# Optimization experiments

Measured on AMD Instinct MI355X. Metric: run time of the kernel, lower is better.

The kernel has to match this reference:

```python
import jax, jax.numpy as jnp
import numpy as np

NUM_CLASSES = 5  # config['training']['num_classes_per_task']


def _conv(x, w, b):
    # x: [N,C,H,W], w: [O,I,kh,kw] (torch OIHW), valid padding, stride 1
    y = jax.lax.conv_general_dilated(
        x, w, window_strides=(1, 1), padding='VALID',
        dimension_numbers=('NCHW', 'OIHW', 'NCHW'))
    return y + b[None, :, None, None]


def _maxpool2(x):
    return jax.lax.reduce_window(x, -jnp.inf, jax.lax.max,
                                 (1, 1, 2, 2), (1, 1, 2, 2), 'VALID')


def _lenet(x, c1w, c1b, c2w, c2b, f1w, f1b, f2w, f2b, f3w, f3b):
    h = _maxpool2(jax.nn.relu(_conv(x, c1w, c1b)))   # [N,6,14,14]
    h = _maxpool2(jax.nn.relu(_conv(h, c2w, c2b)))   # [N,16,5,5]
    h = h.reshape(h.shape[0], -1)                     # [N,400]
    h = jax.nn.relu(h @ f1w.T + f1b)                  # [N,120]
    h = jax.nn.relu(h @ f2w.T + f2b)                  # [N,84]
    return h @ f3w.T + f3b                            # [N,64] embeddings


def setup_inputs() -> dict:
    key = jax.random.key(0)
    ks = jax.random.split(key, 7)
    def w(k, shape, fan_in):
        return jax.random.normal(k, shape, jnp.float32) * (1.0 / np.sqrt(fan_in))
    return {
        'x': jax.random.normal(ks[0], (20480, 3, 32, 32), jnp.float32),
        'c1w': w(ks[1], (6, 3, 5, 5), 3 * 25), 'c1b': jnp.zeros((6,), jnp.float32),
        'c2w': w(ks[2], (16, 6, 5, 5), 6 * 25), 'c2b': jnp.zeros((16,), jnp.float32),
        'f1w': w(ks[3], (120, 400), 400), 'f1b': jnp.zeros((120,), jnp.float32),
        'f2w': w(ks[4], (84, 120), 120), 'f2b': jnp.zeros((84,), jnp.float32),
        'f3w': w(ks[5], (64, 84), 84), 'f3b': jnp.zeros((64,), jnp.float32),
    }


def reference(x, c1w, c1b, c2w, c2b, f1w, f1b, f2w, f2b, f3w, f3b):
    emb = _lenet(x, c1w, c1b, c2w, c2b, f1w, f1b, f2w, f2b, f3w, f3b)  # [N,64]
    # prototypes = embeddings.sum() / num_classes  (scalar, as in source)
    proto = emb.sum() / NUM_CLASSES
    result = jax.nn.softmax(emb, axis=1)
    # sqrt((result - proto)^2) elementwise == |result - proto|; the python
    # per-sample list-comprehension just rebuilds this same [N,64] tensor.
    return jnp.sqrt(jnp.square(result - proto))
```

## Files before the change

kernel.cpp:

```cpp
#include <hip/hip_runtime.h>
#include <math.h>

typedef __attribute__((ext_vector_type(8))) short short8;
typedef __attribute__((ext_vector_type(4))) float f32x4;
typedef __attribute__((ext_vector_type(4))) unsigned short us4v;

__device__ __forceinline__ unsigned short f2bf(float f) {
    unsigned u = __float_as_uint(f);
    return (unsigned short)((u + 0x7FFFu + ((u >> 16) & 1u)) >> 16);
}
__device__ __forceinline__ unsigned cvtpk(float lo, float hi) {
    unsigned r;
    asm("v_cvt_pk_bf16_f32 %0, %1, %2" : "=v"(r) : "v"(lo), "v"(hi));
    return r;
}
__device__ __forceinline__ unsigned short f2bf1(float v) {
    return (unsigned short)(cvtpk(v, 0.f) & 0xffffu);
}
__device__ __forceinline__ float fmax_x8(float v) {
    int s = __builtin_amdgcn_mov_dpp(__float_as_int(v), 0x128, 0xf, 0xf, true);
    return fmaxf(v, __int_as_float(s));
}

#define C1T_SS 3464
#define C1_RS 36
#define P1R 1176

__global__ __launch_bounds__(256, 3) void conv12_mfma(
    const float* __restrict__ x,
    const unsigned short* __restrict__ c1wf, const float* __restrict__ c1b,
    const unsigned short* __restrict__ c2wf, const float* __restrict__ c2b,
    unsigned short* __restrict__ P2)
{
    __shared__ __align__(16) unsigned short img[2 * C1T_SS];
    __shared__ __align__(16) unsigned short p1s[16 * P1R + 16];
    const int t = threadIdx.x;
    const int lane = t & 63, w = t >> 6;
    const int grp = lane >> 4, c = lane & 15;
    const int smp = c >> 3, q = c & 7;

    if (t < 192) {
        int s = t / 96, rr = t - s * 96;
        *(uint2*)&img[s * C1T_SS + rr * C1_RS + 32] = make_uint2(0u, 0u);
    }
    if (t < 2) {
        *(uint4*)&img[t * C1T_SS + 3456] = make_uint4(0u, 0u, 0u, 0u);
        *(uint4*)&p1s[16 * P1R + t * 8] = make_uint4(0u, 0u, 0u, 0u);
    }

    short8 wf1[5][4];
#pragma unroll
    for (int s = 0; s < 5; s++)
#pragma unroll
        for (int off = 0; off < 4; off++)
            wf1[s][off] = *(const short8*)&c1wf[(((s * 4 + off) * 4 + grp) * 16 + c) * 8];
    int ciA[5], kpA[5];
#pragma unroll
    for (int s = 0; s < 5; s++) {
        int b = s * 4 + grp; if (b > 17) b = 17;
        ciA[s] = b / 6; kpA[s] = b % 6;
    }
    const float bias1 = (c < 6) ? c1b[c] : 0.f;

    const float4* xs4 = (const float4*)(x + (size_t)blockIdx.x * 49152);
    float4 r[6];

#pragma unroll
    for (int k = 0; k < 6; k++) r[k] = xs4[k * 256 + t];

    for (int st = 0; st < 8; st++) {
#pragma unroll
        for (int k = 0; k < 6; k++) {
            int f = k * 256 + t;
            int s = (f >= 768) ? 1 : 0;
            int w4 = f - s * 768;
            int ci = w4 >> 8, rem = w4 & 255, y = rem >> 3, xq = rem & 7;
            uint2 pk = make_uint2(cvtpk(r[k].x, r[k].y), cvtpk(r[k].z, r[k].w));
            *(uint2*)&img[s * C1T_SS + (ci * 32 + y) * C1_RS + xq * 4] = pk;
        }
        __syncthreads();

        if (st < 7) {
#pragma unroll
            for (int k = 0; k < 6; k++) r[k] = xs4[(st + 1) * 1536 + k * 256 + t];
        }

        for (int py = w; py < 14; py += 4) {
            f32x4 a00 = {0.f,0.f,0.f,0.f}, a01 = a00, a10 = a00, a11 = a00;
#pragma unroll
            for (int s = 0; s < 5; s++) {
                int e = smp * C1T_SS + (ciA[s] * 32 + py * 2 + kpA[s]) * C1_RS + q * 4;
                union { us4v h[2]; short8 v; } af;
                af.h[0] = *(const us4v*)&img[e];
                af.h[1] = *(const us4v*)&img[e + 4];
                a00 = __builtin_amdgcn_mfma_f32_16x16x32_bf16(af.v, wf1[s][0], a00, 0, 0, 0);
                a01 = __builtin_amdgcn_mfma_f32_16x16x32_bf16(af.v, wf1[s][1], a01, 0, 0, 0);
                a10 = __builtin_amdgcn_mfma_f32_16x16x32_bf16(af.v, wf1[s][2], a10, 0, 0, 0);
                a11 = __builtin_amdgcn_mfma_f32_16x16x32_bf16(af.v, wf1[s][3], a11, 0, 0, 0);
            }
            f32x4 pe2, po2;
#pragma unroll
            for (int i = 0; i < 4; i++) {
                pe2[i] = fmax_x8(fmaxf(a00[i], a01[i]));
                po2[i] = fmax_x8(fmaxf(a10[i], a11[i]));
            }
            if (c < 6) {
#pragma unroll
                for (int i = 0; i < 4; i++) {
                    int m = grp * 4 + i;
                    int qo = m & 7;
                    if (qo < 7) {
                        int sm = m >> 3;
                        float v0 = fmaxf(pe2[i] + bias1, 0.f);
                        float v1 = fmaxf(po2[i] + bias1, 0.f);
                        *(unsigned*)&p1s[(2 * st + sm) * P1R + (c * 14 + py) * 14 + qo * 2]
                            = cvtpk(v0, v1);
                    }
                }
            }
        }
        __syncthreads();
    }

    short8 wf2[8][2];
#pragma unroll
    for (int s = 0; s < 8; s++)
#pragma unroll
        for (int off = 0; off < 2; off++)
            wf2[s][off] = *(const short8*)&c2wf[(((s * 2 + off) * 4 + grp) * 16 + c) * 8];
    int ciB[8], kyB[8];
#pragma unroll
    for (int s = 0; s < 8; s++) {
        int b = s * 4 + grp; if (b > 29) b = 29;
        ciB[s] = b / 5; kyB[s] = b % 5;
    }
    const float bias2 = c2b[c];

    for (int item = w; item < 25; item += 4) {
        int py = item / 5, px = item % 5;
        f32x4 a00 = {0.f,0.f,0.f,0.f}, a01 = a00, a10 = a00, a11 = a00;
#pragma unroll
        for (int s = 0; s < 8; s++) {
            int rbase = ciB[s] * 14 + kyB[s] + py * 2;
#pragma unroll
            for (int yo = 0; yo < 2; yo++) {
                int e = c * P1R + (rbase + yo) * 14 + px * 2;
                union { unsigned u[4]; short8 v; } af;
                af.u[0] = *(const unsigned*)&p1s[e];
                af.u[1] = *(const unsigned*)&p1s[e + 2];
                af.u[2] = *(const unsigned*)&p1s[e + 4];
                af.u[3] = *(const unsigned*)&p1s[e + 6];
                if (yo == 0) {
                    a00 = __builtin_amdgcn_mfma_f32_16x16x32_bf16(af.v, wf2[s][0], a00, 0, 0, 0);
                    a01 = __builtin_amdgcn_mfma_f32_16x16x32_bf16(af.v, wf2[s][1], a01, 0, 0, 0);
                } else {
                    a10 = __builtin_amdgcn_mfma_f32_16x16x32_bf16(af.v, wf2[s][0], a10, 0, 0, 0);
                    a11 = __builtin_amdgcn_mfma_f32_16x16x32_bf16(af.v, wf2[s][1], a11, 0, 0, 0);
                }
            }
        }
#pragma unroll
        for (int i = 0; i < 4; i++) {
            float mx = fmaxf(fmaxf(a00[i], a01[i]), fmaxf(a10[i], a11[i]));
            float v = fmaxf(mx + bias2, 0.f);
            int n = blockIdx.x * 16 + grp * 4 + i;
            P2[(size_t)n * 400 + c * 25 + py * 5 + px] = f2bf1(v);
        }
    }
}

__global__ __launch_bounds__(256) void prep_weights(
    const float* __restrict__ c1w, const float* __restrict__ c2w,
    const float* __restrict__ f1w, const float* __restrict__ f2w,
    const float* __restrict__ f3w,
    unsigned short* __restrict__ wb1, unsigned short* __restrict__ wb2,
    unsigned short* __restrict__ wb3,
    unsigned short* __restrict__ c1wf, unsigned short* __restrict__ c2wf)
{
    const int t0 = blockIdx.x * 256 + threadIdx.x;
    const int stride = gridDim.x * 256;
    for (int i = t0; i < 128 * 416; i += stride) {
        int o = i / 416, k = i % 416;
        wb1[i] = f2bf((o < 120 && k < 400) ? f1w[o * 400 + k] : 0.f);
    }
    for (int i = t0; i < 96 * 128; i += stride) {
        int o = i / 128, k = i % 128;
        wb2[i] = f2bf((o < 84 && k < 120) ? f2w[o * 120 + k] : 0.f);
    }
    for (int i = t0; i < 64 * 96; i += stride) {
        int o = i / 96, k = i % 96;
        wb3[i] = f2bf((k < 84) ? f3w[o * 84 + k] : 0.f);
    }
    for (int i = t0; i < 10240; i += stride) {
        int j = i & 7, c = (i >> 3) & 15, grp = (i >> 7) & 3;
        int off = (i >> 9) & 3, s = i >> 11;
        int b = s * 4 + grp;
        int ci = b / 6, kp = b % 6;
        int kx = j - off;
        float v = 0.f;
        if (b < 18 && kx >= 0 && kx <= 4) {
            if (c < 6 && kp <= 4)
                v = c1w[c * 75 + ci * 25 + kp * 5 + kx];
            else if (c >= 8 && c < 14 && kp >= 1)
                v = c1w[(c - 8) * 75 + ci * 25 + (kp - 1) * 5 + kx];
        }
        c1wf[i] = f2bf(v);
    }
    for (int i = t0; i < 8192; i += stride) {
        int j = i & 7, c = (i >> 3) & 15, grp = (i >> 7) & 3;
        int off = (i >> 9) & 1, s = i >> 10;
        int b = s * 4 + grp;
        int kx = j - off;
        float v = 0.f;
        if (b < 30 && kx >= 0 && kx <= 4) {
            int ci = b / 5, ky = b % 5;
            v = c2w[c * 150 + ci * 25 + ky * 5 + kx];
        }
        c2wf[i] = f2bf(v);
    }
}

#define FCS 32
#define P2S 424
#define A1S 136
#define A2S 104

__global__ __launch_bounds__(256, 3) void fc_mfma(
    const unsigned short* __restrict__ P2,
    const unsigned short* __restrict__ wb1, const float* __restrict__ f1b,
    const unsigned short* __restrict__ wb2, const float* __restrict__ f2b,
    const unsigned short* __restrict__ wb3, const float* __restrict__ f3b,
    float* __restrict__ emb, float* __restrict__ part)
{
    __shared__ __align__(16) unsigned short p2s[FCS * P2S];
    __shared__ __align__(16) unsigned short a1s[FCS * A1S];
    __shared__ __align__(16) unsigned short a2s[FCS * A2S];
    __shared__ float rsum[4];
    const int t = threadIdx.x, lane = t & 63, w = t >> 6;
    const int grp = lane >> 4, c = lane & 15;

    if (t < 64) {
        int s = t >> 1, h = t & 1;
        *(uint4*)&p2s[s * P2S + 400 + h * 8] = make_uint4(0u, 0u, 0u, 0u);
    }
    const uint4* src = (const uint4*)(P2 + (size_t)blockIdx.x * FCS * 400);
    for (int i = t; i < FCS * 50; i += 256) {
        int s = i / 50, k8 = i % 50;
        *(uint4*)&p2s[s * P2S + k8 * 8] = src[i];
    }
    __syncthreads();

    const int m = w & 1;
    const int arow = m * 16 + c;

    {
        const int n0 = (w >> 1) * 4;
        f32x4 acc[4] = {{0.f,0.f,0.f,0.f},{0.f,0.f,0.f,0.f},{0.f,0.f,0.f,0.f},{0.f,0.f,0.f,0.f}};
        const int sb = arow * P2S;
#pragma unroll
        for (int ks = 0; ks < 13; ks++) {
            short8 a = *(const short8*)&p2s[sb + ks * 32 + grp * 8];
#pragma unroll
            for (int j = 0; j < 4; j++) {
                int o = (n0 + j) * 16 + c;
                short8 b = *(const short8*)&wb1[o * 416 + ks * 32 + grp * 8];
                acc[j] = __builtin_amdgcn_mfma_f32_16x16x32_bf16(a, b, acc[j], 0, 0, 0);
            }
        }
#pragma unroll
        for (int j = 0; j < 4; j++) {
            int o = (n0 + j) * 16 + c;
            float bias = (o < 120) ? f1b[o] : 0.f;
#pragma unroll
            for (int i = 0; i < 4; i++) {
                int s = m * 16 + grp * 4 + i;
                a1s[s * A1S + o] = f2bf1(fmaxf(acc[j][i] + bias, 0.f));
            }
        }
    }
    __syncthreads();

    {
        const int n0 = (w >> 1) * 3;
        f32x4 acc[3] = {{0.f,0.f,0.f,0.f},{0.f,0.f,0.f,0.f},{0.f,0.f,0.f,0.f}};
        const int sb = arow * A1S;
#pragma unroll
        for (int ks = 0; ks < 4; ks++) {
            short8 a = *(const short8*)&a1s[sb + ks * 32 + grp * 8];
#pragma unroll
            for (int j = 0; j < 3; j++) {
                int o = (n0 + j) * 16 + c;
                short8 b = *(const short8*)&wb2[o * 128 + ks * 32 + grp * 8];
                acc[j] = __builtin_amdgcn_mfma_f32_16x16x32_bf16(a, b, acc[j], 0, 0, 0);
            }
        }
#pragma unroll
        for (int j = 0; j < 3; j++) {
            int o = (n0 + j) * 16 + c;
            float bias = (o < 84) ? f2b[o] : 0.f;
#pragma unroll
            for (int i = 0; i < 4; i++) {
                int s = m * 16 + grp * 4 + i;
                a2s[s * A2S + o] = f2bf1(fmaxf(acc[j][i] + bias, 0.f));
            }
        }
    }
    __syncthreads();

    {
        const int n0 = (w >> 1) * 2;
        f32x4 acc[2] = {{0.f,0.f,0.f,0.f},{0.f,0.f,0.f,0.f}};
        const int sb = arow * A2S;
#pragma unroll
        for (int ks = 0; ks < 3; ks++) {
            short8 a = *(const short8*)&a2s[sb + ks * 32 + grp * 8];
#pragma unroll
            for (int j = 0; j < 2; j++) {
                int o = (n0 + j) * 16 + c;
                short8 b = *(const short8*)&wb3[o * 96 + ks * 32 + grp * 8];
                acc[j] = __builtin_amdgcn_mfma_f32_16x16x32_bf16(a, b, acc[j], 0, 0, 0);
            }
        }
        float psum = 0.f;
#pragma unroll
        for (int j = 0; j < 2; j++) {
            int o = (n0 + j) * 16 + c;
            float bias = f3b[o];
#pragma unroll
            for (int i = 0; i < 4; i++) {
                int s = m * 16 + grp * 4 + i;
                float v = acc[j][i] + bias;
                emb[((size_t)blockIdx.x * FCS + s) * 64 + o] = v;
                psum += v;
            }
        }
#pragma unroll
        for (int off = 32; off; off >>= 1) psum += __shfl_xor(psum, off);
        if (lane == 0) rsum[w] = psum;
        __syncthreads();
        if (t == 0) part[blockIdx.x] = (rsum[0] + rsum[1]) + (rsum[2] + rsum[3]);
    }
}

__global__ __launch_bounds__(256) void reduce_part(const float* __restrict__ part,
                                                   float* __restrict__ proto) {
    __shared__ float s_[256];
    const int t = threadIdx.x;
    float s = part[t];
    if (t + 256 < 640) s += part[t + 256];
    if (t + 512 < 640) s += part[t + 512];
    s_[t] = s; __syncthreads();
    for (int off = 128; off > 0; off >>= 1) {
        if (t < off) s_[t] += s_[t + off];
        __syncthreads();
    }
    if (t == 0) proto[0] = s_[0] / 5.0f;
}

__global__ __launch_bounds__(256) void softmax_abs(float* __restrict__ io,
                                                   const float* __restrict__ proto_p) {
    const int lane = threadIdx.x & 63;
    const int row = (blockIdx.x << 2) + (threadIdx.x >> 6);
    const float proto = proto_p[0];
    float e = io[(size_t)row * 64 + lane];
    float m = e;
#pragma unroll
    for (int off = 32; off; off >>= 1) m = fmaxf(m, __shfl_xor(m, off));
    float p = expf(e - m);
    float s = p;
#pragma unroll
    for (int off = 32; off; off >>= 1) s += __shfl_xor(s, off);
    io[(size_t)row * 64 + lane] = fabsf(p / s - proto);
}

extern "C" void kernel_launch(void* const* d_in, const int* in_sizes, int n_in,
                              void* d_out, int out_size, void* d_ws, size_t ws_size,
                              hipStream_t stream) {
    const float* x   = (const float*)d_in[0];
    const float* c1w = (const float*)d_in[1];
    const float* c1b = (const float*)d_in[2];
    const float* c2w = (const float*)d_in[3];
    const float* c2b = (const float*)d_in[4];
    const float* f1w = (const float*)d_in[5];
    const float* f1b = (const float*)d_in[6];
    const float* f2w = (const float*)d_in[7];
    const float* f2b = (const float*)d_in[8];
    const float* f3w = (const float*)d_in[9];
    const float* f3b = (const float*)d_in[10];
    float* out = (float*)d_out;

    const int N = in_sizes[0] / 3072;
    const size_t p2_bytes = (size_t)N * 400 * 2;
    unsigned short* P2 = (unsigned short*)d_ws;
    char* tail = (char*)d_ws + p2_bytes;
    float* part  = (float*)tail;
    float* proto = part + 640;
    unsigned short* wb1  = (unsigned short*)(tail + 4096);
    unsigned short* wb2  = wb1 + 128 * 416;
    unsigned short* wb3  = wb2 + 96 * 128;
    unsigned short* c1wf = wb3 + 64 * 96;
    unsigned short* c2wf = c1wf + 10240;

    prep_weights<<<64, 256, 0, stream>>>(c1w, c2w, f1w, f2w, f3w,
                                         wb1, wb2, wb3, c1wf, c2wf);
    conv12_mfma<<<N / 16, 256, 0, stream>>>(x, c1wf, c1b, c2wf, c2b, P2);
    fc_mfma<<<N / 32, 256, 0, stream>>>(P2, wb1, f1b, wb2, f2b, wb3, f3b, out, part);
    reduce_part<<<1, 256, 0, stream>>>(part, proto);
    softmax_abs<<<N / 4, 256, 0, stream>>>(out, proto);
}
```

Baseline: 115.0 us.

## Split conv1/conv2 into two sample groups, double-buffer image, drop reduce kernel

The conv kernel now processes its 16 samples in two groups of 8. It double-buffers the staged input image in LDS, which removes one barrier per stage, and halves the pooled conv1 buffer. Conv2 is remapped so the two pooling rows go into the M dimension of one MFMA pair instead of separate accumulators, giving half the MFMAs per item with wider rows. The separate single-block reduce kernel is removed: each softmax wave sums the 640 partials itself, saving a launch at the cost of redundant reads. Weight fragments are reloaded per group and an extra barrier is added per group.

```diff
diff --git a/kernel.cpp b/kernel.cpp
--- a/kernel.cpp
+++ b/kernel.cpp
@@ -32,140 +32,138 @@
     const unsigned short* __restrict__ c2wf, const float* __restrict__ c2b,
     unsigned short* __restrict__ P2)
 {
-    __shared__ __align__(16) unsigned short img[2 * C1T_SS];
-    __shared__ __align__(16) unsigned short p1s[16 * P1R + 16];
+    __shared__ __align__(16) unsigned short img[4 * C1T_SS];
+    __shared__ __align__(16) unsigned short p1s[8 * P1R + 16];
     const int t = threadIdx.x;
     const int lane = t & 63, w = t >> 6;
     const int grp = lane >> 4, c = lane & 15;
     const int smp = c >> 3, q = c & 7;
 
-    if (t < 192) {
-        int s = t / 96, rr = t - s * 96;
-        *(uint2*)&img[s * C1T_SS + rr * C1_RS + 32] = make_uint2(0u, 0u);
-    }
-    if (t < 2) {
+    for (int rr = t; rr < 384; rr += 256)
+        *(uint2*)&img[(rr / 96) * C1T_SS + (rr % 96) * C1_RS + 32] = make_uint2(0u, 0u);
+    if (t < 4)
         *(uint4*)&img[t * C1T_SS + 3456] = make_uint4(0u, 0u, 0u, 0u);
-        *(uint4*)&p1s[16 * P1R + t * 8] = make_uint4(0u, 0u, 0u, 0u);
-    }
-
-    short8 wf1[5][4];
-#pragma unroll
-    for (int s = 0; s < 5; s++)
-#pragma unroll
-        for (int off = 0; off < 4; off++)
-            wf1[s][off] = *(const short8*)&c1wf[(((s * 4 + off) * 4 + grp) * 16 + c) * 8];
-    int ciA[5], kpA[5];
-#pragma unroll
-    for (int s = 0; s < 5; s++) {
-        int b = s * 4 + grp; if (b > 17) b = 17;
-        ciA[s] = b / 6; kpA[s] = b % 6;
-    }
+    if (t < 2)
+        *(uint4*)&p1s[8 * P1R + t * 8] = make_uint4(0u, 0u, 0u, 0u);
+
     const float bias1 = (c < 6) ? c1b[c] : 0.f;
-
+    const float bias2 = c2b[c];
     const float4* xs4 = (const float4*)(x + (size_t)blockIdx.x * 49152);
     float4 r[6];
 
 #pragma unroll
     for (int k = 0; k < 6; k++) r[k] = xs4[k * 256 + t];
 
-    for (int st = 0; st < 8; st++) {
-#pragma unroll
-        for (int k = 0; k < 6; k++) {
-            int f = k * 256 + t;
-            int s = (f >= 768) ? 1 : 0;
-            int w4 = f - s * 768;
-            int ci = w4 >> 8, rem = w4 & 255, y = rem >> 3, xq = rem & 7;
-            uint2 pk = make_uint2(cvtpk(r[k].x, r[k].y), cvtpk(r[k].z, r[k].w));
-            *(uint2*)&img[s * C1T_SS + (ci * 32 + y) * C1_RS + xq * 4] = pk;
-        }
-        __syncthreads();
-
-        if (st < 7) {
-#pragma unroll
-            for (int k = 0; k < 6; k++) r[k] = xs4[(st + 1) * 1536 + k * 256 + t];
-        }
-
-        for (int py = w; py < 14; py += 4) {
-            f32x4 a00 = {0.f,0.f,0.f,0.f}, a01 = a00, a10 = a00, a11 = a00;
-#pragma unroll
-            for (int s = 0; s < 5; s++) {
-                int e = smp * C1T_SS + (ciA[s] * 32 + py * 2 + kpA[s]) * C1_RS + q * 4;
-                union { us4v h[2]; short8 v; } af;
-                af.h[0] = *(const us4v*)&img[e];
-                af.h[1] = *(const us4v*)&img[e + 4];
-                a00 = __builtin_amdgcn_mfma_f32_16x16x32_bf16(af.v, wf1[s][0], a00, 0, 0, 0);
-                a01 = __builtin_amdgcn_mfma_f32_16x16x32_bf16(af.v, wf1[s][1], a01, 0, 0, 0);
-                a10 = __builtin_amdgcn_mfma_f32_16x16x32_bf16(af.v, wf1[s][2], a10, 0, 0, 0);
-                a11 = __builtin_amdgcn_mfma_f32_16x16x32_bf16(af.v, wf1[s][3], a11, 0, 0, 0);
-            }
-            f32x4 pe2, po2;
-#pragma unroll
-            for (int i = 0; i < 4; i++) {
-                pe2[i] = fmax_x8(fmaxf(a00[i], a01[i]));
-                po2[i] = fmax_x8(fmaxf(a10[i], a11[i]));
-            }
-            if (c < 6) {
+#pragma unroll 1
+    for (int g = 0; g < 2; g++) {
+        short8 wf1[5][4];
+#pragma unroll
+        for (int s = 0; s < 5; s++)
+#pragma unroll
+            for (int off = 0; off < 4; off++)
+                wf1[s][off] = *(const short8*)&c1wf[(((s * 4 + off) * 4 + grp) * 16 + c) * 8];
+        int ciA[5], kpA[5];
+#pragma unroll
+        for (int s = 0; s < 5; s++) {
+            int b = s * 4 + grp; if (b > 17) b = 17;
+            ciA[s] = b / 6; kpA[s] = b % 6;
+        }
+
+#pragma unroll 1
+        for (int st = 0; st < 4; st++) {
+            const int u = g * 4 + st;
+            const int bufo = (u & 1) * (2 * C1T_SS);
+#pragma unroll
+            for (int k = 0; k < 6; k++) {
+                int f = k * 256 + t;
+                int s = (f >= 768) ? 1 : 0;
+                int w4 = f - s * 768;
+                int ci = w4 >> 8, rem = w4 & 255, y = rem >> 3, xq = rem & 7;
+                uint2 pk = make_uint2(cvtpk(r[k].x, r[k].y), cvtpk(r[k].z, r[k].w));
+                *(uint2*)&img[bufo + s * C1T_SS + (ci * 32 + y) * C1_RS + xq * 4] = pk;
+            }
+            __syncthreads();
+
+            if (u < 7) {
+#pragma unroll
+                for (int k = 0; k < 6; k++) r[k] = xs4[(u + 1) * 1536 + k * 256 + t];
+            }
+
+            for (int py = w; py < 14; py += 4) {
+                f32x4 a00 = {0.f,0.f,0.f,0.f}, a01 = a00, a10 = a00, a11 = a00;
+#pragma unroll
+                for (int s = 0; s < 5; s++) {
+                    int e = bufo + smp * C1T_SS + (ciA[s] * 32 + py * 2 + kpA[s]) * C1_RS + q * 4;
+                    union { us4v h[2]; short8 v; } af;
+                    af.h[0] = *(const us4v*)&img[e];
+                    af.h[1] = *(const us4v*)&img[e + 4];
+                    a00 = __builtin_amdgcn_mfma_f32_16x16x32_bf16(af.v, wf1[s][0], a00, 0, 0, 0);
+                    a01 = __builtin_amdgcn_mfma_f32_16x16x32_bf16(af.v, wf1[s][1], a01, 0, 0, 0);
+                    a10 = __builtin_amdgcn_mfma_f32_16x16x32_bf16(af.v, wf1[s][2], a10, 0, 0, 0);
+                    a11 = __builtin_amdgcn_mfma_f32_16x16x32_bf16(af.v, wf1[s][3], a11, 0, 0, 0);
+                }
+                f32x4 pe2, po2;
 #pragma unroll
                 for (int i = 0; i < 4; i++) {
-                    int m = grp * 4 + i;
-                    int qo = m & 7;
-                    if (qo < 7) {
-                        int sm = m >> 3;
-                        float v0 = fmaxf(pe2[i] + bias1, 0.f);
-                        float v1 = fmaxf(po2[i] + bias1, 0.f);
-                        *(unsigned*)&p1s[(2 * st + sm) * P1R + (c * 14 + py) * 14 + qo * 2]
-                            = cvtpk(v0, v1);
+                    pe2[i] = fmax_x8(fmaxf(a00[i], a01[i]));
+                    po2[i] = fmax_x8(fmaxf(a10[i], a11[i]));
+                }
+                if (c < 6) {
+#pragma unroll
+                    for (int i = 0; i < 4; i++) {
+                        int m = grp * 4 + i;
+                        int qo = m & 7;
+                        if (qo < 7) {
+                            int sm = m >> 3;
+                            float v0 = fmaxf(pe2[i] + bias1, 0.f);
+                            float v1 = fmaxf(po2[i] + bias1, 0.f);
+                            *(unsigned*)&p1s[(2 * st + sm) * P1R + (c * 14 + py) * 14 + qo * 2]
+                                = cvtpk(v0, v1);
+                        }
                     }
                 }
             }
         }
+
+        short8 wf2[8][2];
+#pragma unroll
+        for (int s = 0; s < 8; s++)
+#pragma unroll
+            for (int off = 0; off < 2; off++)
+                wf2[s][off] = *(const short8*)&c2wf[(((s * 2 + off) * 4 + grp) * 16 + c) * 8];
+        int ciB[8], kyB[8];
+#pragma unroll
+        for (int s = 0; s < 8; s++) {
+            int b = s * 4 + grp; if (b > 29) b = 29;
+            ciB[s] = b / 5; kyB[s] = b % 5;
+        }
         __syncthreads();
-    }
-
-    short8 wf2[8][2];
-#pragma unroll
-    for (int s = 0; s < 8; s++)
-#pragma unroll
-        for (int off = 0; off < 2; off++)
-            wf2[s][off] = *(const short8*)&c2wf[(((s * 2 + off) * 4 + grp) * 16 + c) * 8];
-    int ciB[8], kyB[8];
-#pragma unroll
-    for (int s = 0; s < 8; s++) {
-        int b = s * 4 + grp; if (b > 29) b = 29;
-        ciB[s] = b / 5; kyB[s] = b % 5;
-    }
-    const float bias2 = c2b[c];
-
-    for (int item = w; item < 25; item += 4) {
-        int py = item / 5, px = item % 5;
-        f32x4 a00 = {0.f,0.f,0.f,0.f}, a01 = a00, a10 = a00, a11 = a00;
-#pragma unroll
-        for (int s = 0; s < 8; s++) {
-            int rbase = ciB[s] * 14 + kyB[s] + py * 2;
-#pragma unroll
-            for (int yo = 0; yo < 2; yo++) {
-                int e = c * P1R + (rbase + yo) * 14 + px * 2;
+
+        const int arow = (c >> 1) * P1R;
+        const int yoff = c & 1;
+        for (int item = w; item < 25; item += 4) {
+            int py = item / 5, px = item % 5;
+            f32x4 a0 = {0.f,0.f,0.f,0.f}, a1 = a0;
+#pragma unroll
+            for (int s = 0; s < 8; s++) {
+                int e = arow + (ciB[s] * 14 + py * 2 + yoff + kyB[s]) * 14 + px * 2;
                 union { unsigned u[4]; short8 v; } af;
                 af.u[0] = *(const unsigned*)&p1s[e];
                 af.u[1] = *(const unsigned*)&p1s[e + 2];
                 af.u[2] = *(const unsigned*)&p1s[e + 4];
                 af.u[3] = *(const unsigned*)&p1s[e + 6];
-                if (yo == 0) {
-                    a00 = __builtin_amdgcn_mfma_f32_16x16x32_bf16(af.v, wf2[s][0], a00, 0, 0, 0);
-                    a01 = __builtin_amdgcn_mfma_f32_16x16x32_bf16(af.v, wf2[s][1], a01, 0, 0, 0);
-                } else {
-                    a10 = __builtin_amdgcn_mfma_f32_16x16x32_bf16(af.v, wf2[s][0], a10, 0, 0, 0);
-                    a11 = __builtin_amdgcn_mfma_f32_16x16x32_bf16(af.v, wf2[s][1], a11, 0, 0, 0);
-                }
-            }
-        }
-#pragma unroll
-        for (int i = 0; i < 4; i++) {
-            float mx = fmaxf(fmaxf(a00[i], a01[i]), fmaxf(a10[i], a11[i]));
-            float v = fmaxf(mx + bias2, 0.f);
-            int n = blockIdx.x * 16 + grp * 4 + i;
-            P2[(size_t)n * 400 + c * 25 + py * 5 + px] = f2bf1(v);
-        }
+                a0 = __builtin_amdgcn_mfma_f32_16x16x32_bf16(af.v, wf2[s][0], a0, 0, 0, 0);
+                a1 = __builtin_amdgcn_mfma_f32_16x16x32_bf16(af.v, wf2[s][1], a1, 0, 0, 0);
+            }
+            float v0 = fmaxf(fmaxf(a0[0], a0[1]), fmaxf(a1[0], a1[1]));
+            float v1 = fmaxf(fmaxf(a0[2], a0[3]), fmaxf(a1[2], a1[3]));
+            v0 = fmaxf(v0 + bias2, 0.f);
+            v1 = fmaxf(v1 + bias2, 0.f);
+            size_t n0 = (size_t)blockIdx.x * 16 + g * 8 + grp * 2;
+            P2[n0 * 400 + c * 25 + py * 5 + px] = f2bf1(v0);
+            P2[(n0 + 1) * 400 + c * 25 + py * 5 + px] = f2bf1(v1);
+        }
+        __syncthreads();
     }
 }
 
@@ -342,27 +340,17 @@
     }
 }
 
-__global__ __launch_bounds__(256) void reduce_part(const float* __restrict__ part,
-                                                   float* __restrict__ proto) {
-    __shared__ float s_[256];
-    const int t = threadIdx.x;
-    float s = part[t];
-    if (t + 256 < 640) s += part[t + 256];
-    if (t + 512 < 640) s += part[t + 512];
-    s_[t] = s; __syncthreads();
-    for (int off = 128; off > 0; off >>= 1) {
-        if (t < off) s_[t] += s_[t + off];
-        __syncthreads();
-    }
-    if (t == 0) proto[0] = s_[0] / 5.0f;
-}
-
 __global__ __launch_bounds__(256) void softmax_abs(float* __restrict__ io,
-                                                   const float* __restrict__ proto_p) {
+                                                   const float* __restrict__ part) {
     const int lane = threadIdx.x & 63;
     const int row = (blockIdx.x << 2) + (threadIdx.x >> 6);
-    const float proto = proto_p[0];
     float e = io[(size_t)row * 64 + lane];
+    float ps = 0.f;
+#pragma unroll
+    for (int k = 0; k < 10; k++) ps += part[k * 64 + lane];
+#pragma unroll
+    for (int off = 32; off; off >>= 1) ps += __shfl_xor(ps, off);
+    const float proto = ps / 5.0f;
     float m = e;
 #pragma unroll
     for (int off = 32; off; off >>= 1) m = fmaxf(m, __shfl_xor(m, off));
@@ -394,7 +382,6 @@
     unsigned short* P2 = (unsigned short*)d_ws;
     char* tail = (char*)d_ws + p2_bytes;
     float* part  = (float*)tail;
-    float* proto = part + 640;
     unsigned short* wb1  = (unsigned short*)(tail + 4096);
     unsigned short* wb2  = wb1 + 128 * 416;
     unsigned short* wb3  = wb2 + 96 * 128;
@@ -405,6 +392,5 @@
                                          wb1, wb2, wb3, c1wf, c2wf);
     conv12_mfma<<<N / 16, 256, 0, stream>>>(x, c1wf, c1b, c2wf, c2b, P2);
     fc_mfma<<<N / 32, 256, 0, stream>>>(P2, wb1, f1b, wb2, f2b, wb3, f3b, out, part);
-    reduce_part<<<1, 256, 0, stream>>>(part, proto);
-    softmax_abs<<<N / 4, 256, 0, stream>>>(out, proto);
-}
+    softmax_abs<<<N / 4, 256, 0, stream>>>(out, part);
+}
```

Measured after the change: 246.9 us. +114.8%, slower.

## Stage conv2 output in LDS for coalesced stores and fold proto reduction into softmax

Applied to the files above, without the earlier changes.

Conv2 results are packed to bf16 pairs in registers, written transposed into shared memory (reusing the p1 buffer), and then copied to global as contiguous 16-byte vectors per block, replacing scattered 2-byte global stores. The separate single-block reduce_part launch is removed; each softmax wave now sums the 640 partials itself, trading one launch and its serialization for redundant small reads in every wave. This adds two extra barriers in conv and depends on p1s being large enough to hold 6400 shorts.

```diff
diff --git a/kernel.cpp b/kernel.cpp
--- a/kernel.cpp
+++ b/kernel.cpp
@@ -136,37 +136,60 @@
     }
     const float bias2 = c2b[c];
 
-    for (int item = w; item < 25; item += 4) {
-        int py = item / 5, px = item % 5;
-        f32x4 a00 = {0.f,0.f,0.f,0.f}, a01 = a00, a10 = a00, a11 = a00;
-#pragma unroll
-        for (int s = 0; s < 8; s++) {
-            int rbase = ciB[s] * 14 + kyB[s] + py * 2;
-#pragma unroll
-            for (int yo = 0; yo < 2; yo++) {
-                int e = c * P1R + (rbase + yo) * 14 + px * 2;
-                union { unsigned u[4]; short8 v; } af;
-                af.u[0] = *(const unsigned*)&p1s[e];
-                af.u[1] = *(const unsigned*)&p1s[e + 2];
-                af.u[2] = *(const unsigned*)&p1s[e + 4];
-                af.u[3] = *(const unsigned*)&p1s[e + 6];
-                if (yo == 0) {
-                    a00 = __builtin_amdgcn_mfma_f32_16x16x32_bf16(af.v, wf2[s][0], a00, 0, 0, 0);
-                    a01 = __builtin_amdgcn_mfma_f32_16x16x32_bf16(af.v, wf2[s][1], a01, 0, 0, 0);
-                } else {
-                    a10 = __builtin_amdgcn_mfma_f32_16x16x32_bf16(af.v, wf2[s][0], a10, 0, 0, 0);
-                    a11 = __builtin_amdgcn_mfma_f32_16x16x32_bf16(af.v, wf2[s][1], a11, 0, 0, 0);
+    unsigned pkbuf[7][2];
+#pragma unroll
+    for (int j = 0; j < 7; j++) {
+        const int item = w + j * 4;
+        if (item < 25) {
+            const int py = item / 5, px = item % 5;
+            f32x4 a00 = {0.f,0.f,0.f,0.f}, a01 = a00, a10 = a00, a11 = a00;
+#pragma unroll
+            for (int s = 0; s < 8; s++) {
+                int rbase = ciB[s] * 14 + kyB[s] + py * 2;
+#pragma unroll
+                for (int yo = 0; yo < 2; yo++) {
+                    int e = c * P1R + (rbase + yo) * 14 + px * 2;
+                    union { unsigned u[4]; short8 v; } af;
+                    af.u[0] = *(const unsigned*)&p1s[e];
+                    af.u[1] = *(const unsigned*)&p1s[e + 2];
+                    af.u[2] = *(const unsigned*)&p1s[e + 4];
+                    af.u[3] = *(const unsigned*)&p1s[e + 6];
+                    if (yo == 0) {
+                        a00 = __builtin_amdgcn_mfma_f32_16x16x32_bf16(af.v, wf2[s][0], a00, 0, 0, 0);
+                        a01 = __builtin_amdgcn_mfma_f32_16x16x32_bf16(af.v, wf2[s][1], a01, 0, 0, 0);
+                    } else {
+                        a10 = __builtin_amdgcn_mfma_f32_16x16x32_bf16(af.v, wf2[s][0], a10, 0, 0, 0);
+                        a11 = __builtin_amdgcn_mfma_f32_16x16x32_bf16(af.v, wf2[s][1], a11, 0, 0, 0);
+                    }
                 }
             }
-        }
-#pragma unroll
-        for (int i = 0; i < 4; i++) {
-            float mx = fmaxf(fmaxf(a00[i], a01[i]), fmaxf(a10[i], a11[i]));
-            float v = fmaxf(mx + bias2, 0.f);
-            int n = blockIdx.x * 16 + grp * 4 + i;
-            P2[(size_t)n * 400 + c * 25 + py * 5 + px] = f2bf1(v);
-        }
-    }
+            float v0 = fmaxf(fmaxf(fmaxf(a00[0], a01[0]), fmaxf(a10[0], a11[0])) + bias2, 0.f);
+            float v1 = fmaxf(fmaxf(fmaxf(a00[1], a01[1]), fmaxf(a10[1], a11[1])) + bias2, 0.f);
+            float v2 = fmaxf(fmaxf(fmaxf(a00[2], a01[2]), fmaxf(a10[2], a11[2])) + bias2, 0.f);
+            float v3 = fmaxf(fmaxf(fmaxf(a00[3], a01[3]), fmaxf(a10[3], a11[3])) + bias2, 0.f);
+            pkbuf[j][0] = cvtpk(v0, v1);
+            pkbuf[j][1] = cvtpk(v2, v3);
+        }
+    }
+    __syncthreads();
+
+    unsigned short* p2t = p1s;
+#pragma unroll
+    for (int j = 0; j < 7; j++) {
+        const int item = w + j * 4;
+        if (item < 25) {
+#pragma unroll
+            for (int i = 0; i < 4; i++) {
+                unsigned v = pkbuf[j][i >> 1] >> ((i & 1) * 16);
+                p2t[(grp * 4 + i) * 400 + c * 25 + item] = (unsigned short)v;
+            }
+        }
+    }
+    __syncthreads();
+
+    uint4* dst = (uint4*)(P2 + (size_t)blockIdx.x * 6400);
+    const uint4* srcT = (const uint4*)p2t;
+    for (int e = t; e < 800; e += 256) dst[e] = srcT[e];
 }
 
 __global__ __launch_bounds__(256) void prep_weights(
@@ -342,27 +365,17 @@
     }
 }
 
-__global__ __launch_bounds__(256) void reduce_part(const float* __restrict__ part,
-                                                   float* __restrict__ proto) {
-    __shared__ float s_[256];
-    const int t = threadIdx.x;
-    float s = part[t];
-    if (t + 256 < 640) s += part[t + 256];
-    if (t + 512 < 640) s += part[t + 512];
-    s_[t] = s; __syncthreads();
-    for (int off = 128; off > 0; off >>= 1) {
-        if (t < off) s_[t] += s_[t + off];
-        __syncthreads();
-    }
-    if (t == 0) proto[0] = s_[0] / 5.0f;
-}
-
 __global__ __launch_bounds__(256) void softmax_abs(float* __restrict__ io,
-                                                   const float* __restrict__ proto_p) {
+                                                   const float* __restrict__ part) {
     const int lane = threadIdx.x & 63;
     const int row = (blockIdx.x << 2) + (threadIdx.x >> 6);
-    const float proto = proto_p[0];
     float e = io[(size_t)row * 64 + lane];
+    float ps = 0.f;
+#pragma unroll
+    for (int k = 0; k < 10; k++) ps += part[k * 64 + lane];
+#pragma unroll
+    for (int off = 32; off; off >>= 1) ps += __shfl_xor(ps, off);
+    const float proto = ps / 5.0f;
     float m = e;
 #pragma unroll
     for (int off = 32; off; off >>= 1) m = fmaxf(m, __shfl_xor(m, off));
@@ -394,7 +407,6 @@
     unsigned short* P2 = (unsigned short*)d_ws;
     char* tail = (char*)d_ws + p2_bytes;
     float* part  = (float*)tail;
-    float* proto = part + 640;
     unsigned short* wb1  = (unsigned short*)(tail + 4096);
     unsigned short* wb2  = wb1 + 128 * 416;
     unsigned short* wb3  = wb2 + 96 * 128;
@@ -405,6 +417,5 @@
                                          wb1, wb2, wb3, c1wf, c2wf);
     conv12_mfma<<<N / 16, 256, 0, stream>>>(x, c1wf, c1b, c2wf, c2b, P2);
     fc_mfma<<<N / 32, 256, 0, stream>>>(P2, wb1, f1b, wb2, f2b, wb3, f3b, out, part);
-    reduce_part<<<1, 256, 0, stream>>>(part, proto);
-    softmax_abs<<<N / 4, 256, 0, stream>>>(out, proto);
-}
+    softmax_abs<<<N / 4, 256, 0, stream>>>(out, part);
+}
```

Measured after the change: 106.7 us. -7.2%, faster.
